# Performance work log

Measured on AMD Instinct MI355X. Metric: run time of the kernel, lower is better.

The kernel has to match this reference:

```python
import jax, jax.numpy as jnp
import numpy as np

B, S, H = 1, 2048, 2048
NH, NKV, HD = 32, 4, 128
G = NH // NKV            # query groups per kv head
EPS = 1e-6
THETA = 1000000.0


def _rmsnorm(x, w):
    # per-head RMSNorm over last (head_dim) axis
    var = jnp.mean(jnp.square(x), axis=-1, keepdims=True)
    return x * jax.lax.rsqrt(var + EPS) * w


def _rotate_half(x):
    x1, x2 = jnp.split(x, 2, axis=-1)
    return jnp.concatenate([-x2, x1], axis=-1)


def _rope(x, cos, sin):
    # x: [B,S,h,HD], cos/sin: [S,HD]
    c = cos[None, :, None, :]
    s = sin[None, :, None, :]
    return x * c + _rotate_half(x) * s


def setup_inputs() -> dict:
    key = jax.random.key(0)
    ks = jax.random.split(key, 7)
    inv_freq = 1.0 / (THETA ** (jnp.arange(0, HD, 2, dtype=jnp.float32) / HD))
    freqs = jnp.outer(jnp.arange(S, dtype=jnp.float32), inv_freq)  # [S, HD/2]
    emb = jnp.concatenate([freqs, freqs], axis=-1)                 # [S, HD]
    std = 0.02
    return {
        "hidden_states": jax.random.normal(ks[0], (B, S, H), jnp.float32),
        "wq": jax.random.normal(ks[1], (H, NH * HD), jnp.float32) * std,
        "wk": jax.random.normal(ks[2], (H, NKV * HD), jnp.float32) * std,
        "wv": jax.random.normal(ks[3], (H, NKV * HD), jnp.float32) * std,
        "wo": jax.random.normal(ks[4], (NH * HD, H), jnp.float32) * std,
        "q_norm_w": jnp.ones((HD,), jnp.float32),
        "k_norm_w": jnp.ones((HD,), jnp.float32),
        "cos": jnp.cos(emb),
        "sin": jnp.sin(emb),
    }


def reference(hidden_states, wq, wk, wv, wo, q_norm_w, k_norm_w, cos, sin):
    b, s, _ = hidden_states.shape
    q = (hidden_states @ wq).reshape(b, s, NH, HD)
    k = (hidden_states @ wk).reshape(b, s, NKV, HD)
    v = (hidden_states @ wv).reshape(b, s, NKV, HD)
    # QK per-head RMSNorm, then interleaved RoPE (rotate-half form)
    q = _rope(_rmsnorm(q, q_norm_w), cos, sin)
    k = _rope(_rmsnorm(k, k_norm_w), cos, sin)
    # GQA: group Q heads per KV head instead of materializing repeated K/V
    qg = q.reshape(b, s, NKV, G, HD)
    scaling = HD ** -0.5
    scores = jnp.einsum('bqhgd,bkhd->bhgqk', qg, k) * scaling  # [B,NKV,G,S,S]
    causal = jnp.tril(jnp.ones((s, s), bool))
    scores = jnp.where(causal, scores, jnp.finfo(scores.dtype).min)
    p = jax.nn.softmax(scores, axis=-1)
    attn = jnp.einsum('bhgqk,bkhd->bqhgd', p, v).reshape(b, s, NH * HD)
    return attn @ wo
```

## Files before the change

### kernel.cpp

```cpp
#include <hip/hip_runtime.h>
#include <hip/hip_bf16.h>
#include <stdint.h>

#define SEQ 2048
#define HDIM 128
#define NHEADS 32
#define NKVH 4

typedef unsigned short u16;
typedef __bf16 bf16_t;
typedef bf16_t bf16x8 __attribute__((ext_vector_type(8)));
typedef float floatx4 __attribute__((ext_vector_type(4)));

__device__ __forceinline__ float bf2f(u16 u) {
  union { uint32_t i; float f; } v; v.i = ((uint32_t)u) << 16; return v.f;
}
__device__ __forceinline__ u16 f2bf(float f) {
  if (__builtin_isnan(f)) return 0;
  union { float f; uint32_t i; } v; v.f = f;
  uint32_t r = v.i + 0x7fffu + ((v.i >> 16) & 1u);
  return (u16)(r >> 16);
}
__device__ __forceinline__ float loadf_any(const void* p, size_t i, int isbf) {
  return isbf ? bf2f(((const u16*)p)[i]) : ((const float*)p)[i];
}

__device__ __forceinline__ void gload_lds16(const u16* g, u16* l) {
  __builtin_amdgcn_global_load_lds((__attribute__((address_space(1))) void*)g,
                                   (__attribute__((address_space(3))) void*)l,
                                   16, 0, 0);
}

__device__ __forceinline__ floatx4 mfma16(bf16x8 a, bf16x8 b, floatx4 c) {
  return __builtin_amdgcn_mfma_f32_16x16x32_bf16(a, b, c, 0, 0, 0);
}

struct InPack { const u16* p[9]; int n[9]; };

__global__ void detect_all(InPack pk, int* __restrict__ flags) {
  const int which = blockIdx.x;
  const u16* x = pk.p[which];
  const int n = pk.n[which];
  __shared__ int s_sane, s_zeven, s_zodd;
  if (threadIdx.x == 0) { s_sane = 0; s_zeven = 0; s_zodd = 0; }
  __syncthreads();
  const int ns = n < 8192 ? n : 8192;
  int sane = 0, zeven = 0, zodd = 0;
  for (int i = threadIdx.x; i < ns; i += 256) {
    const u16 u = x[i];
    const int e = (u >> 7) & 0xff;
    if ((e >= 96 && e <= 159) || u == 0) sane++;
    if (u == 0) { if (i & 1) zodd++; else zeven++; }
  }
#pragma unroll
  for (int off = 32; off >= 1; off >>= 1) {
    sane += __shfl_xor(sane, off, 64);
    zeven += __shfl_xor(zeven, off, 64);
    zodd += __shfl_xor(zodd, off, 64);
  }
  if ((threadIdx.x & 63) == 0) {
    atomicAdd(&s_sane, sane);
    atomicAdd(&s_zeven, zeven);
    atomicAdd(&s_zodd, zodd);
  }
  __syncthreads();
  if (threadIdx.x == 0) {
    const int even = (ns + 1) / 2, odd = ns / 2;
    const bool mostly_sane = (s_sane * 10 >= ns * 9);
    const bool fp32_const_pattern = (s_zeven * 2 >= even) && (s_zodd * 10 <= odd);
    flags[which] = (mostly_sane && !fp32_const_pattern) ? 1 : 0;
    if (which == 0) flags[15] = 1;
  }
}

__global__ __launch_bounds__(256) void convert_any(
    const void* __restrict__ in, u16* __restrict__ out, int n,
    const int* __restrict__ flag) {
  const int isbf = *flag;
  const int i = blockIdx.x * 256 + threadIdx.x;
  if (i >= n) return;
  out[i] = isbf ? ((const u16*)in)[i] : f2bf(((const float*)in)[i]);
}

__global__ __launch_bounds__(256) void transpose_any(
    const void* __restrict__ in, u16* __restrict__ out, int R, int C,
    const int* __restrict__ flag) {
  __shared__ u16 tile[64][65];
  const int isbf = *flag;
  const int c0 = blockIdx.x * 64, r0 = blockIdx.y * 64;
  const int t = threadIdx.x;
#pragma unroll
  for (int i = 0; i < 16; i++) {
    const int idx = i * 256 + t;
    const int r = idx >> 6, c = idx & 63;
    tile[r][c] = (u16)(isbf ? ((const u16*)in)[(size_t)(r0 + r) * C + c0 + c]
                            : f2bf(((const float*)in)[(size_t)(r0 + r) * C + c0 + c]));
  }
  __syncthreads();
#pragma unroll
  for (int i = 0; i < 16; i++) {
    const int idx = i * 256 + t;
    const int cc = idx >> 6, rr = idx & 63;
    out[(size_t)(c0 + cc) * R + r0 + rr] = tile[rr][cc];
  }
}

__global__ __launch_bounds__(256) void gemm_bt_bf16(
    const u16* __restrict__ A, const u16* __restrict__ BT,
    void* __restrict__ C, int M, int N, int K,
    const int* __restrict__ cflag) {
  __shared__ alignas(16) u16 As[128 * 32];
  __shared__ alignas(16) u16 Bs[128 * 32];
  const int t = threadIdx.x;
  const int w = t >> 6;
  const int lane = t & 63;
  const int lhi = lane >> 4, llo = lane & 15;
  const int m0 = blockIdx.y * 128, n0 = blockIdx.x * 128;
  const int wm = (w & 1) * 64, wn = (w >> 1) * 64;

  floatx4 acc[4][4];
#pragma unroll
  for (int i = 0; i < 4; i++)
#pragma unroll
    for (int j = 0; j < 4; j++) acc[i][j] = (floatx4)(0.0f);

  for (int k0 = 0; k0 < K; k0 += 32) {
#pragma unroll
    for (int r = 0; r < 2; r++) {
      const int c = r * 256 + t;
      const int row = c >> 2, kc = c & 3;
      const int base = (r * 256 + w * 64) * 8;
      gload_lds16(A + (size_t)(m0 + row) * K + k0 + kc * 8, &As[base]);
      gload_lds16(BT + (size_t)(n0 + row) * K + k0 + kc * 8, &Bs[base]);
    }
    __syncthreads();
    bf16x8 af[4], bfr[4];
#pragma unroll
    for (int i = 0; i < 4; i++)
      af[i] = *(const bf16x8*)&As[(wm + i * 16 + llo) * 32 + lhi * 8];
#pragma unroll
    for (int j = 0; j < 4; j++)
      bfr[j] = *(const bf16x8*)&Bs[(wn + j * 16 + llo) * 32 + lhi * 8];
#pragma unroll
    for (int i = 0; i < 4; i++)
#pragma unroll
      for (int j = 0; j < 4; j++)
        acc[i][j] = mfma16(af[i], bfr[j], acc[i][j]);
    __syncthreads();
  }
  const int cbf = *cflag;
#pragma unroll
  for (int i = 0; i < 4; i++) {
    const int row0 = m0 + wm + i * 16 + lhi * 4;
#pragma unroll
    for (int j = 0; j < 4; j++) {
      const int col = n0 + wn + j * 16 + llo;
#pragma unroll
      for (int r = 0; r < 4; r++) {
        if (cbf) ((u16*)C)[(size_t)(row0 + r) * N + col] = f2bf(acc[i][j][r]);
        else ((float*)C)[(size_t)(row0 + r) * N + col] = acc[i][j][r];
      }
    }
  }
}

__global__ __launch_bounds__(128) void norm_rope_inplace(
    u16* __restrict__ QKV,
    const void* __restrict__ qw, const void* __restrict__ kw,
    const void* __restrict__ cosb, const void* __restrict__ sinb,
    const int* __restrict__ flags) {
  const int qwbf = flags[5], kwbf = flags[6], cbf = flags[7], sbf = flags[8];
  const int s = blockIdx.x, hy = blockIdx.y, d = threadIdx.x;
  const bool isQ = hy < NHEADS;
  const int col = isQ ? hy * HDIM : 4096 + (hy - NHEADS) * HDIM;
  u16* ptr = QKV + (size_t)s * 5120 + col + d;
  const float x = bf2f(*ptr);
  float v = x * x;
#pragma unroll
  for (int off = 32; off >= 1; off >>= 1) v += __shfl_xor(v, off, 64);
  __shared__ float sw[2];
  __shared__ float sh[128];
  if ((d & 63) == 0) sw[d >> 6] = v;
  __syncthreads();
  const float mean = (sw[0] + sw[1]) * (1.0f / 128.0f);
  const float rn = rsqrtf(mean + 1e-6f);
  const float wv = isQ ? loadf_any(qw, d, qwbf) : loadf_any(kw, d, kwbf);
  const float xn = x * rn * wv;
  sh[d] = xn;
  __syncthreads();
  const float other = sh[d ^ 64];
  const float cv = loadf_any(cosb, (size_t)s * HDIM + d, cbf);
  const float sv = loadf_any(sinb, (size_t)s * HDIM + d, sbf);
  const float o = xn * cv + (d < 64 ? -other : other) * sv;
  *ptr = f2bf(o);
}

__global__ __launch_bounds__(256) void v_transpose(
    const u16* __restrict__ QKV, u16* __restrict__ Vt) {
  __shared__ u16 tile[64][65];
  const int s0 = blockIdx.x * 64, d0 = blockIdx.y * 64, hk = blockIdx.z;
  const int t = threadIdx.x;
#pragma unroll
  for (int i = 0; i < 16; i++) {
    const int idx = i * 256 + t;
    const int r = idx >> 6, c = idx & 63;
    tile[r][c] = QKV[(size_t)(s0 + r) * 5120 + 4608 + hk * HDIM + d0 + c];
  }
  __syncthreads();
#pragma unroll
  for (int i = 0; i < 16; i++) {
    const int idx = i * 256 + t;
    const int dd = idx >> 6, ss = idx & 63;
    Vt[((size_t)hk * HDIM + d0 + dd) * SEQ + s0 + ss] = tile[ss][dd];
  }
}

__global__ __launch_bounds__(256) void flash_attn(
    const u16* __restrict__ QKV, const u16* __restrict__ Vt,
    u16* __restrict__ O) {
  __shared__ alignas(16) u16 Klds[64 * 128];
  __shared__ alignas(16) u16 Vlds[128 * 64];
  __shared__ alignas(16) u16 Plds[4][32 * 72];
  const int t = threadIdx.x;
  const int w = t >> 6;
  const int lane = t & 63;
  const int lhi = lane >> 4, llo = lane & 15;
  const int b = blockIdx.x;
  const int qt = (SEQ / 128 - 1) - (b >> 5);
  const int h = b & 31, hk = h >> 3;
  const int q0 = qt * 128;
  const int qw0 = q0 + w * 32;
  const float scale = 0.08838834764831845f;
  const float SMAX = 16.0f;

  bf16x8 qf[2][4];
#pragma unroll
  for (int i = 0; i < 2; i++)
#pragma unroll
    for (int c = 0; c < 4; c++)
      qf[i][c] = *(const bf16x8*)(QKV + (size_t)(qw0 + i * 16 + llo) * 5120 +
                                  h * HDIM + c * 32 + lhi * 8);

  floatx4 oacc[2][8];
  float lacc[2][4];
#pragma unroll
  for (int i = 0; i < 2; i++) {
#pragma unroll
    for (int d = 0; d < 8; d++) oacc[i][d] = (floatx4)(0.0f);
#pragma unroll
    for (int r = 0; r < 4; r++) lacc[i][r] = 0.0f;
  }

  const int ntiles = 2 * qt + 2;
  for (int tt = 0; tt < ntiles; tt++) {
    const int kv0 = tt * 64;
#pragma unroll
    for (int r = 0; r < 4; r++) {
      const int c = r * 256 + t;
      const int base = (r * 256 + w * 64) * 8;
      gload_lds16(QKV + (size_t)(kv0 + (c >> 4)) * 5120 + 4096 + hk * HDIM +
                      (((c & 15) ^ ((c >> 4) & 7)) * 8),
                  &Klds[base]);
      gload_lds16(Vt + ((size_t)hk * HDIM + (c >> 3)) * SEQ + kv0 +
                      (((c & 7) ^ ((c >> 3) & 7)) * 8),
                  &Vlds[base]);
    }
    __syncthreads();

    floatx4 sacc[2][4];
#pragma unroll
    for (int i = 0; i < 2; i++)
#pragma unroll
      for (int j = 0; j < 4; j++) sacc[i][j] = (floatx4)(0.0f);
#pragma unroll
    for (int j = 0; j < 4; j++) {
#pragma unroll
      for (int c = 0; c < 4; c++) {
        bf16x8 kf = *(const bf16x8*)&Klds[(j * 16 + llo) * 128 +
                                          (((c * 4 + lhi) ^ (llo & 7)) * 8)];
        sacc[0][j] = mfma16(qf[0][c], kf, sacc[0][j]);
        sacc[1][j] = mfma16(qf[1][c], kf, sacc[1][j]);
      }
    }
    if (kv0 + 64 > q0) {
#pragma unroll
      for (int i = 0; i < 2; i++)
#pragma unroll
        for (int j = 0; j < 4; j++) {
          const int n = kv0 + j * 16 + llo;
#pragma unroll
          for (int r = 0; r < 4; r++) {
            const int mm = qw0 + i * 16 + lhi * 4 + r;
            if (n > mm) sacc[i][j][r] = -30000.0f;
          }
        }
    }
#pragma unroll
    for (int i = 0; i < 2; i++)
#pragma unroll
      for (int j = 0; j < 4; j++)
#pragma unroll
        for (int r = 0; r < 4; r++) {
          const float p = __expf(fmaf(sacc[i][j][r], scale, -SMAX));
          lacc[i][r] += p;
          Plds[w][(i * 16 + lhi * 4 + r) * 72 + j * 16 + llo] = f2bf(p);
        }
    asm volatile("" ::: "memory");
    __builtin_amdgcn_s_waitcnt(0);
    asm volatile("" ::: "memory");
#pragma unroll
    for (int c = 0; c < 2; c++) {
      bf16x8 pf0 = *(const bf16x8*)&Plds[w][llo * 72 + c * 32 + lhi * 8];
      bf16x8 pf1 = *(const bf16x8*)&Plds[w][(16 + llo) * 72 + c * 32 + lhi * 8];
#pragma unroll
      for (int d = 0; d < 8; d++) {
        bf16x8 vf = *(const bf16x8*)&Vlds[(d * 16 + llo) * 64 +
                                          (((c * 4 + lhi) ^ (llo & 7)) * 8)];
        oacc[0][d] = mfma16(pf0, vf, oacc[0][d]);
        oacc[1][d] = mfma16(pf1, vf, oacc[1][d]);
      }
    }
    __syncthreads();
  }
#pragma unroll
  for (int i = 0; i < 2; i++)
#pragma unroll
    for (int r = 0; r < 4; r++) {
#pragma unroll
      for (int off = 1; off < 16; off <<= 1)
        lacc[i][r] += __shfl_xor(lacc[i][r], off, 64);
      const float linv = 1.0f / lacc[i][r];
      const int row = qw0 + i * 16 + lhi * 4 + r;
#pragma unroll
      for (int d = 0; d < 8; d++)
        O[(size_t)row * 4096 + h * HDIM + d * 16 + llo] =
            f2bf(oacc[i][d][r] * linv);
    }
}

extern "C" void kernel_launch(void* const* d_in, const int* in_sizes, int n_in,
                              void* d_out, int out_size, void* d_ws, size_t ws_size,
                              hipStream_t stream) {
  char* ws = (char*)d_ws;
  u16* wqkvT  = (u16*)(ws);
  u16* QKVp   = (u16*)(ws + (20ull << 20));
  u16* Vt     = (u16*)(ws + (40ull << 20));
  int* flags  = (int*)(ws + (42ull << 20));
  u16* attnO  = wqkvT;
  u16* woT    = QKVp;
  u16* Hb     = (u16*)d_out;

  InPack pk;
  for (int i = 0; i < 9; i++) { pk.p[i] = (const u16*)d_in[i]; pk.n[i] = in_sizes[i]; }
  detect_all<<<9, 256, 0, stream>>>(pk, flags);

  convert_any<<<(2048 * 2048) / 256, 256, 0, stream>>>(d_in[0], Hb, 2048 * 2048, flags + 0);
  transpose_any<<<dim3(64, 32), 256, 0, stream>>>(d_in[1], wqkvT, 2048, 4096, flags + 1);
  transpose_any<<<dim3(8, 32), 256, 0, stream>>>(d_in[2], wqkvT + 4096ull * 2048, 2048, 512, flags + 2);
  transpose_any<<<dim3(8, 32), 256, 0, stream>>>(d_in[3], wqkvT + 4608ull * 2048, 2048, 512, flags + 3);

  gemm_bt_bf16<<<dim3(40, 16), 256, 0, stream>>>(
      Hb, wqkvT, QKVp, 2048, 5120, 2048, flags + 15);

  norm_rope_inplace<<<dim3(2048, NHEADS + NKVH), 128, 0, stream>>>(
      QKVp, d_in[5], d_in[6], d_in[7], d_in[8], flags);
  v_transpose<<<dim3(32, 2, 4), 256, 0, stream>>>(QKVp, Vt);

  flash_attn<<<512, 256, 0, stream>>>(QKVp, Vt, attnO);

  transpose_any<<<dim3(32, 64), 256, 0, stream>>>(d_in[4], woT, 4096, 2048, flags + 4);
  gemm_bt_bf16<<<dim3(16, 16), 256, 0, stream>>>(
      attnO, woT, d_out, 2048, 2048, 4096, flags + 0);
}
```

Before: 455.0 us.

## Add 256x256-tile pipelined GEMM with 4-stage LDS ring for QKV projection

Adds a new GEMM kernel for the QKV projection. It uses 256x256 output tiles, 512 threads and a four-deep shared-memory ring filled by direct global-to-LDS loads. Each K step is split into two halves with barriers, explicit vmcnt/lgkmcnt waits and raised wave priority around the MFMA bursts, and block IDs are swizzled for L2 locality. The aim is to overlap loads with matrix math and reuse more data per tile than the old 128-tile kernel. In exchange it uses more LDS and registers and launches only 160 blocks.

```diff
diff --git a/kernel.cpp b/kernel.cpp
--- a/kernel.cpp
+++ b/kernel.cpp
@@ -162,6 +162,132 @@
       }
     }
   }
+}
+
+template <int VM, bool STG>
+__device__ __forceinline__ void hstep256(
+    u16 (&As)[4][8192], u16 (&Bs)[4][8192],
+    const u16* __restrict__ gA, const u16* __restrict__ gB,
+    size_t hstep, int ldst, int aoff, int boff, int h,
+    floatx4 (&acc)[2][4][4]) {
+  const int s = h & 3;
+  const int sn = (h + 3) & 3;
+  bf16x8 bf[4], af[4];
+#pragma unroll
+  for (int cf = 0; cf < 4; cf++)
+    bf[cf] = *(const bf16x8*)&Bs[s][boff + cf * 512];
+#pragma unroll
+  for (int rf = 0; rf < 4; rf++)
+    af[rf] = *(const bf16x8*)&As[s][aoff + rf * 512];
+  if (STG) {
+    const size_t g = (size_t)(h + 3) * 32;
+    gload_lds16(gA + g, &As[sn][ldst]);
+    gload_lds16(gA + hstep + g, &As[sn][ldst + 4096]);
+  }
+  __builtin_amdgcn_s_barrier();
+  asm volatile("s_waitcnt lgkmcnt(0)" ::: "memory");
+  __builtin_amdgcn_s_setprio(1);
+#pragma unroll
+  for (int rf = 0; rf < 4; rf++)
+#pragma unroll
+    for (int cf = 0; cf < 4; cf++)
+      acc[0][rf][cf] = mfma16(af[rf], bf[cf], acc[0][rf][cf]);
+  __builtin_amdgcn_s_setprio(0);
+  __builtin_amdgcn_s_barrier();
+#pragma unroll
+  for (int rf = 0; rf < 4; rf++)
+    af[rf] = *(const bf16x8*)&As[s][aoff + 2048 + rf * 512];
+  if (STG) {
+    const size_t g = (size_t)(h + 3) * 32;
+    gload_lds16(gB + g, &Bs[sn][ldst]);
+    gload_lds16(gB + hstep + g, &Bs[sn][ldst + 4096]);
+  }
+  if (VM == 8) asm volatile("s_waitcnt vmcnt(8)" ::: "memory");
+  else if (VM == 4) asm volatile("s_waitcnt vmcnt(4)" ::: "memory");
+  else if (VM == 0) asm volatile("s_waitcnt vmcnt(0)" ::: "memory");
+  __builtin_amdgcn_s_barrier();
+  asm volatile("s_waitcnt lgkmcnt(0)" ::: "memory");
+  __builtin_amdgcn_s_setprio(1);
+#pragma unroll
+  for (int rf = 0; rf < 4; rf++)
+#pragma unroll
+    for (int cf = 0; cf < 4; cf++)
+      acc[1][rf][cf] = mfma16(af[rf], bf[cf], acc[1][rf][cf]);
+  __builtin_amdgcn_s_setprio(0);
+  __builtin_amdgcn_s_barrier();
+}
+
+__global__ __launch_bounds__(512, 2) void gemm_bt_256(
+    const u16* __restrict__ A, const u16* __restrict__ BT,
+    void* __restrict__ C, int M, int N, int K,
+    const int* __restrict__ cflag) {
+  __shared__ alignas(16) u16 As[4][8192];
+  __shared__ alignas(16) u16 Bs[4][8192];
+  const int t = threadIdx.x;
+  const int lane = t & 63;
+  const int wid = t >> 6;
+  const int llo = lane & 15, lhi = lane >> 4;
+  const int wm = (wid >> 2) * 128, wn = (wid & 3) * 64;
+
+  const int nbm = M >> 8, nbn = N >> 8;
+  const int q = (nbm * nbn) >> 3;
+  const int swz = (blockIdx.x & 7) * q + (blockIdx.x >> 3);
+  const int m0 = (swz % nbm) * 256, n0 = (swz / nbm) * 256;
+
+  const int trow = t >> 2;
+  const int cL8 = (((t & 3) ^ ((t >> 3) & 3))) * 8;
+  const int ldst = t * 8;
+  const u16* gA = A + (size_t)(m0 + trow) * K + cL8;
+  const u16* gB = BT + (size_t)(n0 + trow) * K + cL8;
+  const size_t hstep = (size_t)128 * K;
+
+  const int rsw = (lhi ^ ((llo >> 1) & 3)) * 8;
+  const int aoff = (wm + llo) * 32 + rsw;
+  const int boff = (wn + llo) * 32 + rsw;
+
+  floatx4 acc[2][4][4];
+#pragma unroll
+  for (int qd = 0; qd < 2; qd++)
+#pragma unroll
+    for (int i = 0; i < 4; i++)
+#pragma unroll
+      for (int j = 0; j < 4; j++) acc[qd][i][j] = (floatx4)(0.0f);
+
+  const int NH = K >> 5;
+#pragma unroll
+  for (int h = 0; h < 3; h++) {
+    const size_t g = (size_t)h * 32;
+    gload_lds16(gA + g, &As[h][ldst]);
+    gload_lds16(gA + hstep + g, &As[h][ldst + 4096]);
+    gload_lds16(gB + g, &Bs[h][ldst]);
+    gload_lds16(gB + hstep + g, &Bs[h][ldst + 4096]);
+  }
+  asm volatile("s_waitcnt vmcnt(8)" ::: "memory");
+  __builtin_amdgcn_s_barrier();
+
+  int h = 0;
+  for (; h < NH - 3; h++)
+    hstep256<8, true>(As, Bs, gA, gB, hstep, ldst, aoff, boff, h, acc);
+  hstep256<4, false>(As, Bs, gA, gB, hstep, ldst, aoff, boff, h, acc); h++;
+  hstep256<0, false>(As, Bs, gA, gB, hstep, ldst, aoff, boff, h, acc); h++;
+  hstep256<-1, false>(As, Bs, gA, gB, hstep, ldst, aoff, boff, h, acc);
+
+  const int cbf = *cflag;
+#pragma unroll
+  for (int qd = 0; qd < 2; qd++)
+#pragma unroll
+    for (int rf = 0; rf < 4; rf++) {
+      const int row0 = m0 + wm + qd * 64 + rf * 16 + lhi * 4;
+#pragma unroll
+      for (int cf = 0; cf < 4; cf++) {
+        const int col = n0 + wn + cf * 16 + llo;
+#pragma unroll
+        for (int r = 0; r < 4; r++) {
+          if (cbf) ((u16*)C)[(size_t)(row0 + r) * N + col] = f2bf(acc[qd][rf][cf][r]);
+          else ((float*)C)[(size_t)(row0 + r) * N + col] = acc[qd][rf][cf][r];
+        }
+      }
+    }
 }
 
 __global__ __launch_bounds__(128) void norm_rope_inplace(
@@ -359,7 +485,7 @@
   transpose_any<<<dim3(8, 32), 256, 0, stream>>>(d_in[2], wqkvT + 4096ull * 2048, 2048, 512, flags + 2);
   transpose_any<<<dim3(8, 32), 256, 0, stream>>>(d_in[3], wqkvT + 4608ull * 2048, 2048, 512, flags + 3);
 
-  gemm_bt_bf16<<<dim3(40, 16), 256, 0, stream>>>(
+  gemm_bt_256<<<160, 512, 0, stream>>>(
       Hb, wqkvT, QKVp, 2048, 5120, 2048, flags + 15);
 
   norm_rope_inplace<<<dim3(2048, NHEADS + NKVH), 128, 0, stream>>>(
```

Measured after the change: 463.5 us. Within noise of the previous version (+1.9%).
